# Kernel optimization log

Hardware: AMD Instinct MI355X
Metric: run time of the kernel (lower is better)

## Reference

```python
import jax, jax.numpy as jnp
import numpy as np

ROPE_BASE = 10000.0


def _rope_tables(T, d, dtype):
    # inv_freq over even indices, emb = concat(freqs, freqs) -> [T, d]
    inv_freq = 1.0 / (ROPE_BASE ** (jnp.arange(0, d, 2, dtype=jnp.float32) / d))
    t = jnp.arange(T, dtype=jnp.float32)
    freqs = jnp.einsum('i,j->ij', t, inv_freq)          # [T, d/2]
    emb = jnp.concatenate([freqs, freqs], axis=-1)      # [T, d]
    return jnp.cos(emb).astype(dtype), jnp.sin(emb).astype(dtype)


def _rotate_half(x):
    d = x.shape[-1] // 2
    return jnp.concatenate([-x[..., d:], x[..., :d]], axis=-1)


def _apply_rope(x, cos, sin):
    # x: [B, T, H, Dh]; cos/sin: [T, Dh] broadcast over batch and heads
    c = cos[None, :, None, :]
    s = sin[None, :, None, :]
    return x * c + _rotate_half(x) * s


def setup_inputs() -> dict:
    key = jax.random.key(0)
    k1, k2, k3 = jax.random.split(key, 3)
    B, T, C = 2, 2048, 1024
    x = jax.random.normal(k1, (B, T, C), dtype=jnp.float32)
    # weights stored as [in, out] (transposed nn.Linear), scaled like torch init
    W_qkv = jax.random.normal(k2, (C, 3 * C), dtype=jnp.float32) * (C ** -0.5)
    W_proj = jax.random.normal(k3, (C, C), dtype=jnp.float32) * (C ** -0.5)
    return {'x': x, 'W_qkv': W_qkv, 'W_proj': W_proj}


def reference(x, W_qkv, W_proj):
    B, T, C = x.shape
    H = 16
    Dh = C // H
    qkv = x @ W_qkv                                   # [B, T, 3C]
    q, k, v = jnp.split(qkv, 3, axis=-1)
    q = q.reshape(B, T, H, Dh)
    k = k.reshape(B, T, H, Dh)
    v = v.reshape(B, T, H, Dh)
    cos, sin = _rope_tables(T, Dh, x.dtype)
    q = _apply_rope(q, cos, sin)
    k = _apply_rope(k, cos, sin)
    scale = 1.0 / jnp.sqrt(jnp.asarray(Dh, dtype=x.dtype))
    # causal SDPA: scores [B, H, T, T]
    scores = jnp.einsum('bqhd,bkhd->bhqk', q, k) * scale
    causal = jnp.tril(jnp.ones((T, T), dtype=bool))
    scores = jnp.where(causal[None, None], scores, jnp.asarray(-jnp.inf, dtype=scores.dtype))
    attn = jax.nn.softmax(scores, axis=-1)
    y = jnp.einsum('bhqk,bkhd->bqhd', attn, v).reshape(B, T, C)
    return y @ W_proj
```

## Files before the change

kernel.cpp:

```cpp
#include <hip/hip_runtime.h>
#include <cstdint>
#include <cstddef>

typedef __bf16 bf16;
typedef __bf16 bf16x2 __attribute__((ext_vector_type(2)));
typedef __bf16 bf16x4 __attribute__((ext_vector_type(4)));
typedef __bf16 bf16x8 __attribute__((ext_vector_type(8)));
typedef float  f32x4  __attribute__((ext_vector_type(4)));
typedef float  f32x16 __attribute__((ext_vector_type(16)));
typedef int    i32x4  __attribute__((ext_vector_type(4)));

#define G2L(src, dst)                                                          \
  __builtin_amdgcn_global_load_lds(                                            \
      (const __attribute__((address_space(1))) unsigned int*)(src),            \
      (__attribute__((address_space(3))) unsigned int*)(dst), 16, 0, 0)

__global__ void k_f32_to_bf16(const float* __restrict__ in, bf16* __restrict__ out, int n) {
  int i = (blockIdx.x * blockDim.x + threadIdx.x) * 8;
  if (i >= n) return;
  float4 a = *(const float4*)(in + i);
  float4 b = *(const float4*)(in + i + 4);
  bf16x8 o;
  o[0] = (bf16)a.x; o[1] = (bf16)a.y; o[2] = (bf16)a.z; o[3] = (bf16)a.w;
  o[4] = (bf16)b.x; o[5] = (bf16)b.y; o[6] = (bf16)b.z; o[7] = (bf16)b.w;
  *(bf16x8*)(out + i) = o;
}

__global__ void k_transpose_f32_bf16(const float* __restrict__ in, bf16* __restrict__ out,
                                     int R, int C) {
  __shared__ float tile[32][33];
  int c0 = blockIdx.x * 32, r0 = blockIdx.y * 32;
  int tx = threadIdx.x & 31, ty = threadIdx.x >> 5;
#pragma unroll
  for (int i = 0; i < 32; i += 8)
    tile[ty + i][tx] = in[(size_t)(r0 + ty + i) * C + c0 + tx];
  __syncthreads();
#pragma unroll
  for (int i = 0; i < 32; i += 8)
    out[(size_t)(c0 + ty + i) * R + r0 + tx] = (bf16)tile[tx][ty + i];
}

__global__ void k_rope_tables(float* __restrict__ cosT, float* __restrict__ sinT, int total) {
  int i = blockIdx.x * blockDim.x + threadIdx.x;
  if (i >= total) return;
  int t = i >> 5, j = i & 31;
  float inv = powf(10000.0f, -(float)j * (1.0f / 32.0f));
  float f = (float)t * inv;
  cosT[i] = cosf(f);
  sinT[i] = sinf(f);
}

__global__ void k_rope_qk(const bf16* __restrict__ qkv, const float* __restrict__ cosT,
                          const float* __restrict__ sinT, bf16* __restrict__ qr,
                          bf16* __restrict__ kr) {
  int i = blockIdx.x * blockDim.x + threadIdx.x;
  int j = i & 31;
  int h = (i >> 5) & 15;
  int t = (i >> 9) & 2047;
  int b = i >> 20;
  size_t base = (size_t)(b * 2048 + t) * 3072;
  float c = cosT[t * 32 + j], s = sinT[t * 32 + j];
  float qlo = (float)qkv[base + h * 64 + j];
  float qhi = (float)qkv[base + h * 64 + j + 32];
  float klo = (float)qkv[base + 1024 + h * 64 + j];
  float khi = (float)qkv[base + 1024 + h * 64 + j + 32];
  size_t ob = ((size_t)(b * 16 + h) * 2048 + t) * 64;
  qr[ob + j]      = (bf16)((qlo * c - qhi * s) * 0.125f);
  qr[ob + j + 32] = (bf16)((qhi * c + qlo * s) * 0.125f);
  kr[ob + j]      = (bf16)(klo * c - khi * s);
  kr[ob + j + 32] = (bf16)(khi * c + klo * s);
}

__global__ void k_v_scatter(const bf16* __restrict__ qkv, bf16* __restrict__ vt) {
  __shared__ bf16 tile[64][66];
  int bh = blockIdx.y;
  int t0 = blockIdx.x * 64;
  int b = bh >> 4, h = bh & 15;
  int tt = threadIdx.x >> 2, c4 = (threadIdx.x & 3) * 16;
  const bf16* src = qkv + (size_t)(b * 2048 + t0 + tt) * 3072 + 2048 + h * 64 + c4;
  bf16x8 v0 = *(const bf16x8*)src;
  bf16x8 v1 = *(const bf16x8*)(src + 8);
#pragma unroll
  for (int j = 0; j < 8; j++) { tile[tt][c4 + j] = v0[j]; tile[tt][c4 + 8 + j] = v1[j]; }
  __syncthreads();
  int d = threadIdx.x >> 2, tc0 = (threadIdx.x & 3) * 16;
  bf16x8 o0, o1;
#pragma unroll
  for (int j = 0; j < 8; j++) { o0[j] = tile[tc0 + j][d]; o1[j] = tile[tc0 + 8 + j][d]; }
  bf16* dst = vt + ((size_t)bh * 64 + d) * 2048 + t0 + tc0;
  *(bf16x8*)dst = o0;
  *(bf16x8*)(dst + 8) = o1;
}

template <int OUTF32>
__global__ __launch_bounds__(256) void k_gemm_bt(const bf16* __restrict__ A,
                                                 const bf16* __restrict__ Bt,
                                                 float* __restrict__ Cf, bf16* __restrict__ Cb,
                                                 int M, int N, int K) {
  __shared__ __align__(16) bf16 sA[128 * 64];
  __shared__ __align__(16) bf16 sB[128 * 64];
  int m0 = blockIdx.y * 128, n0 = blockIdx.x * 128;
  int t = threadIdx.x, lane = t & 63, w = t >> 6;
  int wr = w >> 1, wc = w & 1;
  int lr = lane & 15, q2 = lane >> 4;
  int srow8 = lane >> 3, pc8 = lane & 7;
  f32x4 acc[4][4] = {};
  for (int k0 = 0; k0 < K; k0 += 64) {
#pragma unroll
    for (int is = 0; is < 4; is++) {
      int r = w * 32 + is * 8 + srow8;
      int lc = pc8 ^ (r & 7);
      G2L(A + (size_t)(m0 + r) * K + k0 + lc * 8, &sA[(w * 32 + is * 8) * 64]);
    }
#pragma unroll
    for (int is = 0; is < 4; is++) {
      int r = w * 32 + is * 8 + srow8;
      int lc = pc8 ^ (r & 7);
      G2L(Bt + (size_t)(n0 + r) * K + k0 + lc * 8, &sB[(w * 32 + is * 8) * 64]);
    }
    __syncthreads();
#pragma unroll
    for (int ch = 0; ch < 2; ch++) {
      bf16x8 af[4], bfr[4];
#pragma unroll
      for (int i = 0; i < 4; i++) {
        int r = wr * 64 + i * 16 + lr;
        af[i] = *(const bf16x8*)&sA[r * 64 + (((ch * 4 + q2) ^ (r & 7)) * 8)];
      }
#pragma unroll
      for (int i = 0; i < 4; i++) {
        int r = wc * 64 + i * 16 + lr;
        bfr[i] = *(const bf16x8*)&sB[r * 64 + (((ch * 4 + q2) ^ (r & 7)) * 8)];
      }
#pragma unroll
      for (int mi = 0; mi < 4; mi++)
#pragma unroll
        for (int ni = 0; ni < 4; ni++)
          acc[mi][ni] = __builtin_amdgcn_mfma_f32_16x16x32_bf16(af[mi], bfr[ni], acc[mi][ni], 0, 0, 0);
    }
    __syncthreads();
  }
  int row_base = m0 + wr * 64, col_base = n0 + wc * 64;
#pragma unroll
  for (int mi = 0; mi < 4; mi++)
#pragma unroll
    for (int ni = 0; ni < 4; ni++) {
      int col = col_base + ni * 16 + lr;
#pragma unroll
      for (int r = 0; r < 4; r++) {
        int row = row_base + mi * 16 + q2 * 4 + r;
        float v = acc[mi][ni][r];
        if (OUTF32) Cf[(size_t)row * N + col] = v;
        else        Cb[(size_t)row * N + col] = (bf16)v;
      }
    }
}

__global__ __launch_bounds__(128) void k_flash(const bf16* __restrict__ qr,
                                               const bf16* __restrict__ kr,
                                               const bf16* __restrict__ vt,
                                               bf16* __restrict__ out) {
  const int T = 2048;
  int id = blockIdx.x;
  int qb = 31 - (id >> 5);
  int bh = id & 31;
  int b = bh >> 4, h = bh & 15;
  __shared__ __align__(16) bf16 sK[2][64 * 64];
  __shared__ __align__(16) bf16 sV[2][64 * 64];
  int t = threadIdx.x, lane = t & 63, w = t >> 6;
  int q31 = lane & 31, hi = lane >> 5;
  int srow8 = lane >> 3, pc8 = lane & 7;

  const bf16* Kbh = kr + (size_t)bh * T * 64;
  const bf16* Vbh = vt + (size_t)bh * 64 * T;

  int nk = qb + 1;
  int qwb = qb * 64 + w * 32;
  int qg = qwb + q31;

  const bf16* qrow = qr + ((size_t)bh * T + qg) * 64 + hi * 8;
  bf16x8 qf[4];
#pragma unroll
  for (int ks = 0; ks < 4; ks++) qf[ks] = *(const bf16x8*)(qrow + ks * 16);
  f32x16 o0 = {}, o1 = {};
  float m = -1e30f, l = 0.f;

  auto stage = [&](int buf, int kt) {
#pragma unroll
    for (int is = 0; is < 4; is++) {
      int r = w * 32 + is * 8 + srow8;
      int lc = pc8 ^ (r & 7);
      G2L(Kbh + (size_t)(kt * 64 + r) * 64 + lc * 8, &sK[buf][(w * 32 + is * 8) * 64]);
    }
#pragma unroll
    for (int is = 0; is < 4; is++) {
      int d = w * 32 + is * 8 + srow8;
      int lc = pc8 ^ (d & 7);
      G2L(Vbh + (size_t)d * T + kt * 64 + lc * 8, &sV[buf][(w * 32 + is * 8) * 64]);
    }
  };

  stage(0, 0);
  for (int kt = 0; kt < nk; kt++) {
    int buf = kt & 1;
    if (kt + 1 < nk) {
      stage(buf ^ 1, kt + 1);
      asm volatile("s_waitcnt vmcnt(8)" ::: "memory");
    } else {
      asm volatile("s_waitcnt vmcnt(0)" ::: "memory");
    }
    __builtin_amdgcn_s_barrier();
    asm volatile("" ::: "memory");
    __builtin_amdgcn_sched_barrier(0);
    const bf16* Kb = &sK[buf][0];
    const bf16* Vb = &sV[buf][0];
    f32x16 s[2];
    __builtin_amdgcn_s_setprio(1);
#pragma unroll
    for (int kb = 0; kb < 2; kb++) {
      f32x16 a = {};
      int krow = kb * 32 + q31;
#pragma unroll
      for (int ks = 0; ks < 4; ks++) {
        int ch = (ks * 2 + hi) ^ (krow & 7);
        bf16x8 kf = *(const bf16x8*)&Kb[krow * 64 + ch * 8];
        a = __builtin_amdgcn_mfma_f32_32x32x16_bf16(kf, qf[ks], a, 0, 0, 0);
      }
      s[kb] = a;
    }
    __builtin_amdgcn_s_setprio(0);
    if (kt == qb) {
      int thr = qg - kt * 64;
#pragma unroll
      for (int kb = 0; kb < 2; kb++)
#pragma unroll
        for (int r = 0; r < 16; r++) {
          int koff = kb * 32 + (r & 3) + 8 * (r >> 2) + 4 * hi;
          if (koff > thr) s[kb][r] = -1e30f;
        }
    }
    float tm[16];
#pragma unroll
    for (int i = 0; i < 16; i++) tm[i] = fmaxf(s[0][i], s[1][i]);
#pragma unroll
    for (int st = 8; st > 0; st >>= 1)
#pragma unroll
      for (int i = 0; i < st; i++) tm[i] = fmaxf(tm[i], tm[i + st]);
    float px = tm[0];
    px = fmaxf(px, __shfl_xor(px, 32, 64));
    float mn = fmaxf(m, px);
    float alpha = __expf(m - mn);
    m = mn;
    float ts[16];
#pragma unroll
    for (int i = 0; i < 16; i++) {
      float p0 = __expf(s[0][i] - m);
      float p1 = __expf(s[1][i] - m);
      s[0][i] = p0;
      s[1][i] = p1;
      ts[i] = p0 + p1;
    }
#pragma unroll
    for (int st = 8; st > 0; st >>= 1)
#pragma unroll
      for (int i = 0; i < st; i++) ts[i] += ts[i + st];
    float rs = ts[0];
    rs += __shfl_xor(rs, 32, 64);
    l = l * alpha + rs;
    int pw[4][4];
#pragma unroll
    for (int kb = 0; kb < 2; kb++) {
      int wd[8];
#pragma unroll
      for (int g = 0; g < 4; g++) {
        bf16x2 a, c;
        a[0] = (bf16)s[kb][4 * g + 0]; a[1] = (bf16)s[kb][4 * g + 1];
        c[0] = (bf16)s[kb][4 * g + 2]; c[1] = (bf16)s[kb][4 * g + 3];
        wd[2 * g]     = __builtin_bit_cast(int, a);
        wd[2 * g + 1] = __builtin_bit_cast(int, c);
      }
      asm volatile("v_permlane32_swap_b32 %0, %1" : "+v"(wd[0]), "+v"(wd[2]));
      asm volatile("v_permlane32_swap_b32 %0, %1" : "+v"(wd[1]), "+v"(wd[3]));
      asm volatile("v_permlane32_swap_b32 %0, %1" : "+v"(wd[4]), "+v"(wd[6]));
      asm volatile("v_permlane32_swap_b32 %0, %1" : "+v"(wd[5]), "+v"(wd[7]));
      pw[2 * kb][0] = wd[0]; pw[2 * kb][1] = wd[1];
      pw[2 * kb][2] = wd[2]; pw[2 * kb][3] = wd[3];
      pw[2 * kb + 1][0] = wd[4]; pw[2 * kb + 1][1] = wd[5];
      pw[2 * kb + 1][2] = wd[6]; pw[2 * kb + 1][3] = wd[7];
    }
#pragma unroll
    for (int r = 0; r < 16; r++) { o0[r] *= alpha; o1[r] *= alpha; }
    __builtin_amdgcn_s_setprio(1);
#pragma unroll
    for (int ks = 0; ks < 4; ks++) {
      i32x4 pv = {pw[ks][0], pw[ks][1], pw[ks][2], pw[ks][3]};
      bf16x8 pb = __builtin_bit_cast(bf16x8, pv);
      {
        int drow = q31;
        int ch = (ks * 2 + hi) ^ (drow & 7);
        bf16x8 vf = *(const bf16x8*)&Vb[drow * 64 + ch * 8];
        o0 = __builtin_amdgcn_mfma_f32_32x32x16_bf16(vf, pb, o0, 0, 0, 0);
      }
      {
        int drow = 32 + q31;
        int ch = (ks * 2 + hi) ^ (drow & 7);
        bf16x8 vf = *(const bf16x8*)&Vb[drow * 64 + ch * 8];
        o1 = __builtin_amdgcn_mfma_f32_32x32x16_bf16(vf, pb, o1, 0, 0, 0);
      }
    }
    __builtin_amdgcn_s_setprio(0);
    asm volatile("" ::: "memory");
    __builtin_amdgcn_s_barrier();
    asm volatile("" ::: "memory");
  }
  float linv = 1.0f / l;
  bf16* orow = out + ((size_t)b * T + qg) * 1024 + h * 64;
#pragma unroll
  for (int g = 0; g < 4; g++) {
    bf16x4 v0, v1;
#pragma unroll
    for (int j = 0; j < 4; j++) {
      v0[j] = (bf16)(o0[4 * g + j] * linv);
      v1[j] = (bf16)(o1[4 * g + j] * linv);
    }
    *(bf16x4*)&orow[8 * g + 4 * hi]      = v0;
    *(bf16x4*)&orow[32 + 8 * g + 4 * hi] = v1;
  }
}

extern "C" void kernel_launch(void* const* d_in, const int* in_sizes, int n_in,
                              void* d_out, int out_size, void* d_ws, size_t ws_size,
                              hipStream_t stream) {
  const float* x     = (const float*)d_in[0];
  const float* Wqkv  = (const float*)d_in[1];
  const float* Wproj = (const float*)d_in[2];
  float* outp = (float*)d_out;
  const int B = 2, T = 2048, C = 1024;
  const int M = B * T;

  char* ws = (char*)d_ws;
  size_t off = 0;
  auto alloc = [&](size_t bytes) {
    void* p = ws + off;
    off += (bytes + 255) & ~(size_t)255;
    return p;
  };
  bf16* xb     = (bf16*)alloc((size_t)M * C * 2);
  bf16* wqkvt  = (bf16*)alloc((size_t)3 * C * C * 2);
  bf16* wprojt = (bf16*)alloc((size_t)C * C * 2);
  float* cosT  = (float*)alloc((size_t)T * 32 * 4);
  float* sinT  = (float*)alloc((size_t)T * 32 * 4);
  bf16* qkv    = (bf16*)alloc((size_t)M * 3 * C * 2);
  bf16* qr     = (bf16*)alloc((size_t)M * C * 2);
  bf16* kr     = (bf16*)alloc((size_t)M * C * 2);
  bf16* vt     = (bf16*)alloc((size_t)M * C * 2);
  bf16* attn   = qkv;

  k_f32_to_bf16<<<dim3(M * C / 8 / 256), dim3(256), 0, stream>>>(x, xb, M * C);
  k_transpose_f32_bf16<<<dim3(3 * C / 32, C / 32), dim3(256), 0, stream>>>(Wqkv, wqkvt, C, 3 * C);
  k_transpose_f32_bf16<<<dim3(C / 32, C / 32), dim3(256), 0, stream>>>(Wproj, wprojt, C, C);
  k_rope_tables<<<dim3(T * 32 / 256), dim3(256), 0, stream>>>(cosT, sinT, T * 32);
  k_gemm_bt<0><<<dim3(3 * C / 128, M / 128), dim3(256), 0, stream>>>(xb, wqkvt, (float*)nullptr, qkv, M, 3 * C, C);
  k_rope_qk<<<dim3((B * T * 16 * 32) / 256), dim3(256), 0, stream>>>(qkv, cosT, sinT, qr, kr);
  k_v_scatter<<<dim3(T / 64, 32), dim3(256), 0, stream>>>(qkv, vt);
  k_flash<<<dim3(1024), dim3(128), 0, stream>>>(qr, kr, vt, attn);
  k_gemm_bt<1><<<dim3(C / 128, M / 128), dim3(256), 0, stream>>>(attn, wprojt, outp, (bf16*)nullptr, M, C, C);
}
```

Measured before the change: 140.8 us.

## Fuse RoPE and V transpose into QKV GEMM epilogue; pair causal blocks in flash

The QKV GEMM epilogue now applies RoPE and the Q scaling directly and writes Q/K in head-major layout and V transposed. This removes the intermediate qkv buffer and the separate rope and scatter kernels. The flash kernel now has each block process a complementary pair of query tiles (qb and 31-qb) to balance causal work. It also software-pipelines the next QK^T product ahead of softmax, with K and V staged separately. The epilogue stores become scattered 2-byte writes, and the flash loop waits on vmcnt(0) every iteration, which may reduce load overlap.

Result: slower. 145.0 us (+3.0%).

```diff
diff --git a/kernel.cpp b/kernel.cpp
--- a/kernel.cpp
+++ b/kernel.cpp
@@ -50,53 +50,99 @@
   sinT[i] = sinf(f);
 }
 
-__global__ void k_rope_qk(const bf16* __restrict__ qkv, const float* __restrict__ cosT,
-                          const float* __restrict__ sinT, bf16* __restrict__ qr,
-                          bf16* __restrict__ kr) {
-  int i = blockIdx.x * blockDim.x + threadIdx.x;
-  int j = i & 31;
-  int h = (i >> 5) & 15;
-  int t = (i >> 9) & 2047;
-  int b = i >> 20;
-  size_t base = (size_t)(b * 2048 + t) * 3072;
-  float c = cosT[t * 32 + j], s = sinT[t * 32 + j];
-  float qlo = (float)qkv[base + h * 64 + j];
-  float qhi = (float)qkv[base + h * 64 + j + 32];
-  float klo = (float)qkv[base + 1024 + h * 64 + j];
-  float khi = (float)qkv[base + 1024 + h * 64 + j + 32];
-  size_t ob = ((size_t)(b * 16 + h) * 2048 + t) * 64;
-  qr[ob + j]      = (bf16)((qlo * c - qhi * s) * 0.125f);
-  qr[ob + j + 32] = (bf16)((qhi * c + qlo * s) * 0.125f);
-  kr[ob + j]      = (bf16)(klo * c - khi * s);
-  kr[ob + j + 32] = (bf16)(khi * c + klo * s);
-}
-
-__global__ void k_v_scatter(const bf16* __restrict__ qkv, bf16* __restrict__ vt) {
-  __shared__ bf16 tile[64][66];
-  int bh = blockIdx.y;
-  int t0 = blockIdx.x * 64;
-  int b = bh >> 4, h = bh & 15;
-  int tt = threadIdx.x >> 2, c4 = (threadIdx.x & 3) * 16;
-  const bf16* src = qkv + (size_t)(b * 2048 + t0 + tt) * 3072 + 2048 + h * 64 + c4;
-  bf16x8 v0 = *(const bf16x8*)src;
-  bf16x8 v1 = *(const bf16x8*)(src + 8);
-#pragma unroll
-  for (int j = 0; j < 8; j++) { tile[tt][c4 + j] = v0[j]; tile[tt][c4 + 8 + j] = v1[j]; }
-  __syncthreads();
-  int d = threadIdx.x >> 2, tc0 = (threadIdx.x & 3) * 16;
-  bf16x8 o0, o1;
-#pragma unroll
-  for (int j = 0; j < 8; j++) { o0[j] = tile[tc0 + j][d]; o1[j] = tile[tc0 + 8 + j][d]; }
-  bf16* dst = vt + ((size_t)bh * 64 + d) * 2048 + t0 + tc0;
-  *(bf16x8*)dst = o0;
-  *(bf16x8*)(dst + 8) = o1;
-}
-
-template <int OUTF32>
-__global__ __launch_bounds__(256) void k_gemm_bt(const bf16* __restrict__ A,
-                                                 const bf16* __restrict__ Bt,
-                                                 float* __restrict__ Cf, bf16* __restrict__ Cb,
-                                                 int M, int N, int K) {
+__global__ __launch_bounds__(256) void k_gemm_qkv(const bf16* __restrict__ A,
+                                                  const bf16* __restrict__ Bt,
+                                                  const float* __restrict__ cosT,
+                                                  const float* __restrict__ sinT,
+                                                  bf16* __restrict__ qr,
+                                                  bf16* __restrict__ kr,
+                                                  bf16* __restrict__ vt) {
+  const int Kd = 1024, T = 2048;
+  __shared__ __align__(16) bf16 sA[128 * 64];
+  __shared__ __align__(16) bf16 sB[128 * 64];
+  int m0 = blockIdx.y * 128, n0 = blockIdx.x * 128;
+  int t = threadIdx.x, lane = t & 63, w = t >> 6;
+  int wr = w >> 1, wc = w & 1;
+  int lr = lane & 15, q2 = lane >> 4;
+  int srow8 = lane >> 3, pc8 = lane & 7;
+  f32x4 acc[4][4] = {};
+  for (int k0 = 0; k0 < Kd; k0 += 64) {
+#pragma unroll
+    for (int is = 0; is < 4; is++) {
+      int r = w * 32 + is * 8 + srow8;
+      int lc = pc8 ^ (r & 7);
+      G2L(A + (size_t)(m0 + r) * Kd + k0 + lc * 8, &sA[(w * 32 + is * 8) * 64]);
+    }
+#pragma unroll
+    for (int is = 0; is < 4; is++) {
+      int r = w * 32 + is * 8 + srow8;
+      int lc = pc8 ^ (r & 7);
+      G2L(Bt + (size_t)(n0 + r) * Kd + k0 + lc * 8, &sB[(w * 32 + is * 8) * 64]);
+    }
+    __syncthreads();
+#pragma unroll
+    for (int ch = 0; ch < 2; ch++) {
+      bf16x8 af[4], bfr[4];
+#pragma unroll
+      for (int i = 0; i < 4; i++) {
+        int r = wr * 64 + i * 16 + lr;
+        af[i] = *(const bf16x8*)&sA[r * 64 + (((ch * 4 + q2) ^ (r & 7)) * 8)];
+      }
+#pragma unroll
+      for (int i = 0; i < 4; i++) {
+        int r = wc * 64 + i * 16 + lr;
+        bfr[i] = *(const bf16x8*)&sB[r * 64 + (((ch * 4 + q2) ^ (r & 7)) * 8)];
+      }
+#pragma unroll
+      for (int mi = 0; mi < 4; mi++)
+#pragma unroll
+        for (int ni = 0; ni < 4; ni++)
+          acc[mi][ni] = __builtin_amdgcn_mfma_f32_16x16x32_bf16(af[mi], bfr[ni], acc[mi][ni], 0, 0, 0);
+    }
+    __syncthreads();
+  }
+  int row_base = m0 + wr * 64, col_base = n0 + wc * 64;
+  int sec = col_base >> 10;
+  int h = (col_base & 1023) >> 6;
+  if (sec < 2) {
+    bf16* dst = (sec == 0) ? qr : kr;
+    float scl = (sec == 0) ? 0.125f : 1.0f;
+#pragma unroll
+    for (int mi = 0; mi < 4; mi++)
+#pragma unroll
+      for (int r = 0; r < 4; r++) {
+        int row = row_base + mi * 16 + q2 * 4 + r;
+        int b = row >> 11, tt = row & 2047;
+        size_t obase = ((size_t)(b * 16 + h) * T + tt) * 64;
+#pragma unroll
+        for (int ni = 0; ni < 2; ni++) {
+          int jl = ni * 16 + lr;
+          float c = cosT[tt * 32 + jl], s = sinT[tt * 32 + jl];
+          float vlo = acc[mi][ni][r], vhi = acc[mi][ni + 2][r];
+          dst[obase + jl]      = (bf16)((vlo * c - vhi * s) * scl);
+          dst[obase + jl + 32] = (bf16)((vhi * c + vlo * s) * scl);
+        }
+      }
+  } else {
+#pragma unroll
+    for (int mi = 0; mi < 4; mi++)
+#pragma unroll
+      for (int ni = 0; ni < 4; ni++) {
+        int j = ni * 16 + lr;
+        int row0 = row_base + mi * 16 + q2 * 4;
+        int b = row0 >> 11, tt = row0 & 2047;
+        bf16x4 pk;
+#pragma unroll
+        for (int r = 0; r < 4; r++) pk[r] = (bf16)acc[mi][ni][r];
+        *(bf16x4*)&vt[((size_t)(b * 16 + h) * 64 + j) * T + tt] = pk;
+      }
+  }
+}
+
+__global__ __launch_bounds__(256) void k_gemm_proj(const bf16* __restrict__ A,
+                                                   const bf16* __restrict__ Bt,
+                                                   float* __restrict__ Cf,
+                                                   int M, int N, int K) {
   __shared__ __align__(16) bf16 sA[128 * 64];
   __shared__ __align__(16) bf16 sB[128 * 64];
   int m0 = blockIdx.y * 128, n0 = blockIdx.x * 128;
@@ -149,9 +195,7 @@
 #pragma unroll
       for (int r = 0; r < 4; r++) {
         int row = row_base + mi * 16 + q2 * 4 + r;
-        float v = acc[mi][ni][r];
-        if (OUTF32) Cf[(size_t)row * N + col] = v;
-        else        Cb[(size_t)row * N + col] = (bf16)v;
+        Cf[(size_t)row * N + col] = acc[mi][ni][r];
       }
     }
 }
@@ -161,9 +205,8 @@
                                                const bf16* __restrict__ vt,
                                                bf16* __restrict__ out) {
   const int T = 2048;
-  int id = blockIdx.x;
-  int qb = 31 - (id >> 5);
-  int bh = id & 31;
+  int pair = blockIdx.x;
+  int bh = blockIdx.y;
   int b = bh >> 4, h = bh & 15;
   __shared__ __align__(16) bf16 sK[2][64 * 64];
   __shared__ __align__(16) bf16 sV[2][64 * 64];
@@ -174,24 +217,15 @@
   const bf16* Kbh = kr + (size_t)bh * T * 64;
   const bf16* Vbh = vt + (size_t)bh * 64 * T;
 
-  int nk = qb + 1;
-  int qwb = qb * 64 + w * 32;
-  int qg = qwb + q31;
-
-  const bf16* qrow = qr + ((size_t)bh * T + qg) * 64 + hi * 8;
-  bf16x8 qf[4];
-#pragma unroll
-  for (int ks = 0; ks < 4; ks++) qf[ks] = *(const bf16x8*)(qrow + ks * 16);
-  f32x16 o0 = {}, o1 = {};
-  float m = -1e30f, l = 0.f;
-
-  auto stage = [&](int buf, int kt) {
+  auto stageK = [&](int buf, int kt) {
 #pragma unroll
     for (int is = 0; is < 4; is++) {
       int r = w * 32 + is * 8 + srow8;
       int lc = pc8 ^ (r & 7);
       G2L(Kbh + (size_t)(kt * 64 + r) * 64 + lc * 8, &sK[buf][(w * 32 + is * 8) * 64]);
     }
+  };
+  auto stageV = [&](int buf, int kt) {
 #pragma unroll
     for (int is = 0; is < 4; is++) {
       int d = w * 32 + is * 8 + srow8;
@@ -200,131 +234,148 @@
     }
   };
 
-  stage(0, 0);
-  for (int kt = 0; kt < nk; kt++) {
-    int buf = kt & 1;
-    if (kt + 1 < nk) {
-      stage(buf ^ 1, kt + 1);
-      asm volatile("s_waitcnt vmcnt(8)" ::: "memory");
-    } else {
-      asm volatile("s_waitcnt vmcnt(0)" ::: "memory");
-    }
+  for (int sel = 0; sel < 2; sel++) {
+    int qb = sel ? (31 - pair) : pair;
+    int nk = qb + 1;
+    int qwb = qb * 64 + w * 32;
+    int qg = qwb + q31;
+    const bf16* qrow = qr + ((size_t)bh * T + qg) * 64 + hi * 8;
+    bf16x8 qf[4];
+#pragma unroll
+    for (int ks = 0; ks < 4; ks++) qf[ks] = *(const bf16x8*)(qrow + ks * 16);
+    f32x16 o0 = {}, o1 = {};
+    float m = -1e30f, l = 0.f;
+
+    auto computeQK = [&](int buf, f32x16* sarr) {
+      const bf16* Kb = &sK[buf][0];
+#pragma unroll
+      for (int kb = 0; kb < 2; kb++) {
+        f32x16 a = {};
+        int krow = kb * 32 + q31;
+#pragma unroll
+        for (int ks = 0; ks < 4; ks++) {
+          int ch = (ks * 2 + hi) ^ (krow & 7);
+          bf16x8 kf = *(const bf16x8*)&Kb[krow * 64 + ch * 8];
+          a = __builtin_amdgcn_mfma_f32_32x32x16_bf16(kf, qf[ks], a, 0, 0, 0);
+        }
+        sarr[kb] = a;
+      }
+    };
+
+    stageK(0, 0);
+    stageV(0, 0);
+    stageK(1, nk > 1 ? 1 : 0);
+    asm volatile("s_waitcnt vmcnt(0)" ::: "memory");
     __builtin_amdgcn_s_barrier();
     asm volatile("" ::: "memory");
-    __builtin_amdgcn_sched_barrier(0);
-    const bf16* Kb = &sK[buf][0];
-    const bf16* Vb = &sV[buf][0];
-    f32x16 s[2];
-    __builtin_amdgcn_s_setprio(1);
-#pragma unroll
-    for (int kb = 0; kb < 2; kb++) {
-      f32x16 a = {};
-      int krow = kb * 32 + q31;
+    f32x16 sc[2];
+    computeQK(0, sc);
+
+    for (int kt = 0; kt < nk; kt++) {
+      int vnext = min(kt + 1, nk - 1);
+      int knext = min(kt + 2, nk - 1);
+      stageV((kt + 1) & 1, vnext);
+      stageK(kt & 1, knext);
+      f32x16 nx[2];
+      bool have_next = (kt + 1 < nk);
+      if (have_next) computeQK((kt + 1) & 1, nx);
+      if (kt == qb) {
+        int thr = qg - kt * 64;
+#pragma unroll
+        for (int kb = 0; kb < 2; kb++)
+#pragma unroll
+          for (int r = 0; r < 16; r++) {
+            int koff = kb * 32 + (r & 3) + 8 * (r >> 2) + 4 * hi;
+            if (koff > thr) sc[kb][r] = -1e30f;
+          }
+      }
+      float tm[16];
+#pragma unroll
+      for (int i = 0; i < 16; i++) tm[i] = fmaxf(sc[0][i], sc[1][i]);
+#pragma unroll
+      for (int st = 8; st > 0; st >>= 1)
+#pragma unroll
+        for (int i = 0; i < st; i++) tm[i] = fmaxf(tm[i], tm[i + st]);
+      float px = tm[0];
+      px = fmaxf(px, __shfl_xor(px, 32, 64));
+      float mn = fmaxf(m, px);
+      float alpha = __expf(m - mn);
+      m = mn;
+      float ts[16];
+#pragma unroll
+      for (int i = 0; i < 16; i++) {
+        float p0 = __expf(sc[0][i] - m);
+        float p1 = __expf(sc[1][i] - m);
+        sc[0][i] = p0;
+        sc[1][i] = p1;
+        ts[i] = p0 + p1;
+      }
+#pragma unroll
+      for (int st = 8; st > 0; st >>= 1)
+#pragma unroll
+        for (int i = 0; i < st; i++) ts[i] += ts[i + st];
+      float rs = ts[0];
+      rs += __shfl_xor(rs, 32, 64);
+      l = l * alpha + rs;
+      int pw[4][4];
+#pragma unroll
+      for (int kb = 0; kb < 2; kb++) {
+        int wd[8];
+#pragma unroll
+        for (int g = 0; g < 4; g++) {
+          bf16x2 a, c;
+          a[0] = (bf16)sc[kb][4 * g + 0]; a[1] = (bf16)sc[kb][4 * g + 1];
+          c[0] = (bf16)sc[kb][4 * g + 2]; c[1] = (bf16)sc[kb][4 * g + 3];
+          wd[2 * g]     = __builtin_bit_cast(int, a);
+          wd[2 * g + 1] = __builtin_bit_cast(int, c);
+        }
+        asm volatile("v_permlane32_swap_b32 %0, %1" : "+v"(wd[0]), "+v"(wd[2]));
+        asm volatile("v_permlane32_swap_b32 %0, %1" : "+v"(wd[1]), "+v"(wd[3]));
+        asm volatile("v_permlane32_swap_b32 %0, %1" : "+v"(wd[4]), "+v"(wd[6]));
+        asm volatile("v_permlane32_swap_b32 %0, %1" : "+v"(wd[5]), "+v"(wd[7]));
+        pw[2 * kb][0] = wd[0]; pw[2 * kb][1] = wd[1];
+        pw[2 * kb][2] = wd[2]; pw[2 * kb][3] = wd[3];
+        pw[2 * kb + 1][0] = wd[4]; pw[2 * kb + 1][1] = wd[5];
+        pw[2 * kb + 1][2] = wd[6]; pw[2 * kb + 1][3] = wd[7];
+      }
+#pragma unroll
+      for (int r = 0; r < 16; r++) { o0[r] *= alpha; o1[r] *= alpha; }
+      const bf16* Vb = &sV[kt & 1][0];
 #pragma unroll
       for (int ks = 0; ks < 4; ks++) {
-        int ch = (ks * 2 + hi) ^ (krow & 7);
-        bf16x8 kf = *(const bf16x8*)&Kb[krow * 64 + ch * 8];
-        a = __builtin_amdgcn_mfma_f32_32x32x16_bf16(kf, qf[ks], a, 0, 0, 0);
-      }
-      s[kb] = a;
-    }
-    __builtin_amdgcn_s_setprio(0);
-    if (kt == qb) {
-      int thr = qg - kt * 64;
-#pragma unroll
-      for (int kb = 0; kb < 2; kb++)
-#pragma unroll
-        for (int r = 0; r < 16; r++) {
-          int koff = kb * 32 + (r & 3) + 8 * (r >> 2) + 4 * hi;
-          if (koff > thr) s[kb][r] = -1e30f;
+        i32x4 pv = {pw[ks][0], pw[ks][1], pw[ks][2], pw[ks][3]};
+        bf16x8 pb = __builtin_bit_cast(bf16x8, pv);
+        {
+          int drow = q31;
+          int ch = (ks * 2 + hi) ^ (drow & 7);
+          bf16x8 vf = *(const bf16x8*)&Vb[drow * 64 + ch * 8];
+          o0 = __builtin_amdgcn_mfma_f32_32x32x16_bf16(vf, pb, o0, 0, 0, 0);
         }
-    }
-    float tm[16];
-#pragma unroll
-    for (int i = 0; i < 16; i++) tm[i] = fmaxf(s[0][i], s[1][i]);
-#pragma unroll
-    for (int st = 8; st > 0; st >>= 1)
-#pragma unroll
-      for (int i = 0; i < st; i++) tm[i] = fmaxf(tm[i], tm[i + st]);
-    float px = tm[0];
-    px = fmaxf(px, __shfl_xor(px, 32, 64));
-    float mn = fmaxf(m, px);
-    float alpha = __expf(m - mn);
-    m = mn;
-    float ts[16];
-#pragma unroll
-    for (int i = 0; i < 16; i++) {
-      float p0 = __expf(s[0][i] - m);
-      float p1 = __expf(s[1][i] - m);
-      s[0][i] = p0;
-      s[1][i] = p1;
-      ts[i] = p0 + p1;
-    }
-#pragma unroll
-    for (int st = 8; st > 0; st >>= 1)
-#pragma unroll
-      for (int i = 0; i < st; i++) ts[i] += ts[i + st];
-    float rs = ts[0];
-    rs += __shfl_xor(rs, 32, 64);
-    l = l * alpha + rs;
-    int pw[4][4];
-#pragma unroll
-    for (int kb = 0; kb < 2; kb++) {
-      int wd[8];
-#pragma unroll
-      for (int g = 0; g < 4; g++) {
-        bf16x2 a, c;
-        a[0] = (bf16)s[kb][4 * g + 0]; a[1] = (bf16)s[kb][4 * g + 1];
-        c[0] = (bf16)s[kb][4 * g + 2]; c[1] = (bf16)s[kb][4 * g + 3];
-        wd[2 * g]     = __builtin_bit_cast(int, a);
-        wd[2 * g + 1] = __builtin_bit_cast(int, c);
-      }
-      asm volatile("v_permlane32_swap_b32 %0, %1" : "+v"(wd[0]), "+v"(wd[2]));
-      asm volatile("v_permlane32_swap_b32 %0, %1" : "+v"(wd[1]), "+v"(wd[3]));
-      asm volatile("v_permlane32_swap_b32 %0, %1" : "+v"(wd[4]), "+v"(wd[6]));
-      asm volatile("v_permlane32_swap_b32 %0, %1" : "+v"(wd[5]), "+v"(wd[7]));
-      pw[2 * kb][0] = wd[0]; pw[2 * kb][1] = wd[1];
-      pw[2 * kb][2] = wd[2]; pw[2 * kb][3] = wd[3];
-      pw[2 * kb + 1][0] = wd[4]; pw[2 * kb + 1][1] = wd[5];
-      pw[2 * kb + 1][2] = wd[6]; pw[2 * kb + 1][3] = wd[7];
-    }
-#pragma unroll
-    for (int r = 0; r < 16; r++) { o0[r] *= alpha; o1[r] *= alpha; }
-    __builtin_amdgcn_s_setprio(1);
-#pragma unroll
-    for (int ks = 0; ks < 4; ks++) {
-      i32x4 pv = {pw[ks][0], pw[ks][1], pw[ks][2], pw[ks][3]};
-      bf16x8 pb = __builtin_bit_cast(bf16x8, pv);
-      {
-        int drow = q31;
-        int ch = (ks * 2 + hi) ^ (drow & 7);
-        bf16x8 vf = *(const bf16x8*)&Vb[drow * 64 + ch * 8];
-        o0 = __builtin_amdgcn_mfma_f32_32x32x16_bf16(vf, pb, o0, 0, 0, 0);
-      }
-      {
-        int drow = 32 + q31;
-        int ch = (ks * 2 + hi) ^ (drow & 7);
-        bf16x8 vf = *(const bf16x8*)&Vb[drow * 64 + ch * 8];
-        o1 = __builtin_amdgcn_mfma_f32_32x32x16_bf16(vf, pb, o1, 0, 0, 0);
-      }
-    }
-    __builtin_amdgcn_s_setprio(0);
-    asm volatile("" ::: "memory");
-    __builtin_amdgcn_s_barrier();
-    asm volatile("" ::: "memory");
-  }
-  float linv = 1.0f / l;
-  bf16* orow = out + ((size_t)b * T + qg) * 1024 + h * 64;
-#pragma unroll
-  for (int g = 0; g < 4; g++) {
-    bf16x4 v0, v1;
-#pragma unroll
-    for (int j = 0; j < 4; j++) {
-      v0[j] = (bf16)(o0[4 * g + j] * linv);
-      v1[j] = (bf16)(o1[4 * g + j] * linv);
-    }
-    *(bf16x4*)&orow[8 * g + 4 * hi]      = v0;
-    *(bf16x4*)&orow[32 + 8 * g + 4 * hi] = v1;
+        {
+          int drow = 32 + q31;
+          int ch = (ks * 2 + hi) ^ (drow & 7);
+          bf16x8 vf = *(const bf16x8*)&Vb[drow * 64 + ch * 8];
+          o1 = __builtin_amdgcn_mfma_f32_32x32x16_bf16(vf, pb, o1, 0, 0, 0);
+        }
+      }
+      if (have_next) { sc[0] = nx[0]; sc[1] = nx[1]; }
+      asm volatile("s_waitcnt vmcnt(0)" ::: "memory");
+      __builtin_amdgcn_s_barrier();
+      asm volatile("" ::: "memory");
+    }
+    float linv = 1.0f / l;
+    bf16* orow = out + ((size_t)b * T + qg) * 1024 + h * 64;
+#pragma unroll
+    for (int g = 0; g < 4; g++) {
+      bf16x4 v0, v1;
+#pragma unroll
+      for (int j = 0; j < 4; j++) {
+        v0[j] = (bf16)(o0[4 * g + j] * linv);
+        v1[j] = (bf16)(o1[4 * g + j] * linv);
+      }
+      *(bf16x4*)&orow[8 * g + 4 * hi]      = v0;
+      *(bf16x4*)&orow[32 + 8 * g + 4 * hi] = v1;
+    }
   }
 }
 
@@ -350,19 +401,16 @@
   bf16* wprojt = (bf16*)alloc((size_t)C * C * 2);
   float* cosT  = (float*)alloc((size_t)T * 32 * 4);
   float* sinT  = (float*)alloc((size_t)T * 32 * 4);
-  bf16* qkv    = (bf16*)alloc((size_t)M * 3 * C * 2);
   bf16* qr     = (bf16*)alloc((size_t)M * C * 2);
   bf16* kr     = (bf16*)alloc((size_t)M * C * 2);
   bf16* vt     = (bf16*)alloc((size_t)M * C * 2);
-  bf16* attn   = qkv;
+  bf16* attn   = (bf16*)alloc((size_t)M * C * 2);
 
   k_f32_to_bf16<<<dim3(M * C / 8 / 256), dim3(256), 0, stream>>>(x, xb, M * C);
   k_transpose_f32_bf16<<<dim3(3 * C / 32, C / 32), dim3(256), 0, stream>>>(Wqkv, wqkvt, C, 3 * C);
   k_transpose_f32_bf16<<<dim3(C / 32, C / 32), dim3(256), 0, stream>>>(Wproj, wprojt, C, C);
   k_rope_tables<<<dim3(T * 32 / 256), dim3(256), 0, stream>>>(cosT, sinT, T * 32);
-  k_gemm_bt<0><<<dim3(3 * C / 128, M / 128), dim3(256), 0, stream>>>(xb, wqkvt, (float*)nullptr, qkv, M, 3 * C, C);
-  k_rope_qk<<<dim3((B * T * 16 * 32) / 256), dim3(256), 0, stream>>>(qkv, cosT, sinT, qr, kr);
-  k_v_scatter<<<dim3(T / 64, 32), dim3(256), 0, stream>>>(qkv, vt);
-  k_flash<<<dim3(1024), dim3(128), 0, stream>>>(qr, kr, vt, attn);
-  k_gemm_bt<1><<<dim3(C / 128, M / 128), dim3(256), 0, stream>>>(attn, wprojt, outp, (bf16*)nullptr, M, C, C);
-}
+  k_gemm_qkv<<<dim3(3 * C / 128, M / 128), dim3(256), 0, stream>>>(xb, wqkvt, cosT, sinT, qr, kr, vt);
+  k_flash<<<dim3(16, 32), dim3(128), 0, stream>>>(qr, kr, vt, attn);
+  k_gemm_proj<<<dim3(C / 128, M / 128), dim3(256), 0, stream>>>(attn, wprojt, outp, M, C, C);
+}
```
